# Kernel tuning notes

Hardware: AMD Instinct MI355X
Metric: run time of the kernel (lower is better)

## Reference

```python
import jax, jax.numpy as jnp
import numpy as np
import math

B, S, HID = 2, 4096, 2048
H, D, C = 16, 128, 256  # heads, head_dim, chunk (block) size
NC = S // C


def _build_slopes(n):
    # faithful port of MiniMaxText01LinearAttention._build_slope_tensor
    def p2(m):
        start = 2.0 ** (-(2.0 ** (-(math.log2(m) - 3))))
        return [start * (start ** i) for i in range(m)]
    if math.log2(n).is_integer():
        sl = p2(n)
    else:
        cp = 2 ** math.floor(math.log2(n))
        sl = p2(cp) + p2(2 * cp)[0::2][: n - cp]
    return np.asarray(sl, dtype=np.float32).reshape(n, 1, 1)


def setup_inputs() -> dict:
    key = jax.random.key(0)
    k1, k2, k3, k4 = jax.random.split(key, 4)
    x = jax.random.normal(k1, (B, S, HID), dtype=jnp.float32)
    w_qkv = jax.random.normal(k2, (HID, 3 * H * D), dtype=jnp.float32) * 0.02
    w_gate = jax.random.normal(k3, (HID, H * D), dtype=jnp.float32) * 0.02
    w_out = jax.random.normal(k4, (H * D, HID), dtype=jnp.float32) * 0.02
    slopes = jnp.asarray(_build_slopes(H))  # [H,1,1]
    return {"x": x, "w_qkv": w_qkv, "w_gate": w_gate, "w_out": w_out, "slopes": slopes}


def _to_chunks(t):
    # [B,S,H*D] -> [NC,B,H,C,D]
    return (t.reshape(B, S, H, D)
             .transpose(0, 2, 1, 3)          # [B,H,S,D]
             .reshape(B, H, NC, C, D)
             .transpose(2, 0, 1, 3, 4))      # [NC,B,H,C,D]


def _lightning_attn(q, k, v, slopes):
    # q,k,v: [NC,B,H,C,D]; slopes: [H,1,1]
    s = slopes
    pos = jnp.arange(C, dtype=jnp.float32)
    q_decay = jnp.exp(-s * (pos + 1.0).reshape(1, C, 1))        # [H,C,1]
    k_decay = jnp.exp(-s * (C - 1.0 - pos).reshape(1, C, 1))    # [H,C,1]
    idx = pos[:, None] - pos[None, :]                            # [C,C]
    diag_decay = jnp.where(idx >= 0, jnp.exp(-s * idx), 0.0)     # [H,C,C]
    block_decay = jnp.exp(-s * float(C))[None]                   # [1,H,1,1]

    def step(kv, qkv_c):
        qc, kc, vc = qkv_c  # each [B,H,C,D]
        # intra-chunk (causal, decayed)
        scores = jnp.einsum('bhid,bhjd->bhij', qc, kc) * diag_decay
        o = jnp.einsum('bhij,bhjd->bhid', scores, vc)
        # inter-chunk via recurrent state kv: [B,H,D,D]
        o = o + jnp.einsum('bhid,bhde->bhie', qc * q_decay, kv)
        kv = block_decay * kv + jnp.einsum('bhjd,bhje->bhde', kc * k_decay, vc)
        return kv, o

    kv0 = jnp.zeros((B, H, D, D), dtype=q.dtype)
    _, outs = jax.lax.scan(step, kv0, (q, k, v))  # outs: [NC,B,H,C,D]
    return (outs.transpose(1, 2, 0, 3, 4)          # [B,H,NC,C,D]
                .reshape(B, H, S, D)
                .transpose(0, 2, 1, 3)
                .reshape(B, S, H * D))


def reference(x, w_qkv, w_gate, w_out, slopes):
    qkv = jax.nn.silu(x @ w_qkv)                   # act on fused qkv (hidden_act=silu)
    q, k, v = jnp.split(qkv, 3, axis=-1)
    attn = _lightning_attn(_to_chunks(q), _to_chunks(k), _to_chunks(v), slopes)
    gate = jax.nn.sigmoid(x @ w_gate)              # output gate
    return (gate * attn) @ w_out
```

## Files before the change

kernel.cpp:

```cpp
#include <hip/hip_runtime.h>

typedef __bf16 bf16;
typedef __bf16 bf16x8 __attribute__((ext_vector_type(8)));
typedef __bf16 bf16x4 __attribute__((ext_vector_type(4)));
typedef float  f32x4  __attribute__((ext_vector_type(4)));

#define B_   2
#define S_   4096
#define HID_ 2048
#define H_   16
#define D_   128
#define C_   256
#define NC_  16
#define M_   (B_*S_)
#define K_   2048

typedef __attribute__((address_space(1))) const void gas_t;
typedef __attribute__((address_space(3))) void las_t;

__global__ void cvt_x_kernel(const float* __restrict__ x, bf16* __restrict__ xb) {
    int idx = (blockIdx.x * 256 + threadIdx.x) * 8;
    float4 f0 = *(const float4*)(x + idx);
    float4 f1 = *(const float4*)(x + idx + 4);
    bf16x8 o;
    o[0] = (bf16)f0.x; o[1] = (bf16)f0.y; o[2] = (bf16)f0.z; o[3] = (bf16)f0.w;
    o[4] = (bf16)f1.x; o[5] = (bf16)f1.y; o[6] = (bf16)f1.z; o[7] = (bf16)f1.w;
    *(bf16x8*)(xb + idx) = o;
}

__global__ void cvt_w_kernel(const float* __restrict__ wqkv,
                             const float* __restrict__ wgate,
                             const float* __restrict__ wout,
                             bf16* __restrict__ wT) {
    __shared__ float tile[32][33];
    int k0 = blockIdx.x * 32, n0 = blockIdx.y * 32;
    const float* src; int ld, col0;
    if (n0 < 6144)      { src = wqkv;  ld = 6144; col0 = n0; }
    else if (n0 < 8192) { src = wgate; ld = 2048; col0 = n0 - 6144; }
    else                { src = wout;  ld = 2048; col0 = n0 - 8192; }
    int tx = threadIdx.x, ty = threadIdx.y;
#pragma unroll
    for (int i = 0; i < 4; i++) {
        int kk = ty + i * 8;
        tile[kk][tx] = src[(size_t)(k0 + kk) * ld + col0 + tx];
    }
    __syncthreads();
#pragma unroll
    for (int i = 0; i < 4; i++) {
        int nn = ty + i * 8;
        wT[(size_t)(n0 + nn) * K_ + k0 + tx] = (bf16)tile[tx][nn];
    }
}

template <int MODE>
__global__ __launch_bounds__(256) void gemm_kernel(
        const bf16* __restrict__ A, const bf16* __restrict__ Bm,
        bf16* __restrict__ qo, bf16* __restrict__ ko,
        bf16* __restrict__ vo, bf16* __restrict__ go,
        float* __restrict__ out) {
    __shared__ __align__(16) bf16 As[128 * 32];
    __shared__ __align__(16) bf16 Bs[128 * 32];
    const int m0 = blockIdx.x * 128, n0 = blockIdx.y * 128;
    const int tid = threadIdx.x, lane = tid & 63, wid = tid >> 6;
    const int quad = lane >> 4, l15 = lane & 15;
    const int i0w = (wid >> 1) * 64, j0w = (wid & 1) * 64;
    f32x4 acc[4][4] = {};
    const int srow = tid >> 2, scol = (tid & 3) * 8;
    const bf16* Ag = A  + (size_t)(m0 + srow) * K_ + scol;
    const bf16* Bg = Bm + (size_t)(n0 + srow) * K_ + scol;
    const size_t rowskip = (size_t)64 * K_;
    bf16* AsDst = As + tid * 8;
    bf16* BsDst = Bs + tid * 8;

    for (int kb = 0; kb < K_; kb += 32) {
        __builtin_amdgcn_global_load_lds((gas_t*)(Ag + kb),           (las_t*)AsDst,          16, 0, 0);
        __builtin_amdgcn_global_load_lds((gas_t*)(Ag + kb + rowskip), (las_t*)(AsDst + 2048), 16, 0, 0);
        __builtin_amdgcn_global_load_lds((gas_t*)(Bg + kb),           (las_t*)BsDst,          16, 0, 0);
        __builtin_amdgcn_global_load_lds((gas_t*)(Bg + kb + rowskip), (las_t*)(BsDst + 2048), 16, 0, 0);
        __syncthreads();
        bf16x8 af[4], bfr[4];
#pragma unroll
        for (int t = 0; t < 4; t++)
            af[t] = *(const bf16x8*)&As[(i0w + t * 16 + l15) * 32 + quad * 8];
#pragma unroll
        for (int t = 0; t < 4; t++)
            bfr[t] = *(const bf16x8*)&Bs[(j0w + t * 16 + l15) * 32 + quad * 8];
#pragma unroll
        for (int ti = 0; ti < 4; ti++)
#pragma unroll
            for (int tj = 0; tj < 4; tj++)
                acc[ti][tj] = __builtin_amdgcn_mfma_f32_16x16x32_bf16(
                    af[ti], bfr[tj], acc[ti][tj], 0, 0, 0);
        __syncthreads();
    }

    if (MODE == 0) {
        bf16* outb = (n0 < 2048) ? qo : (n0 < 4096) ? ko : (n0 < 6144) ? vo : go;
        const bool silu = (n0 < 6144);
        const int cb = n0 & 2047;
#pragma unroll
        for (int ti = 0; ti < 4; ti++)
#pragma unroll
            for (int tj = 0; tj < 4; tj++)
#pragma unroll
                for (int r = 0; r < 4; r++) {
                    int row = m0 + i0w + ti * 16 + quad * 4 + r;
                    int col = cb + j0w + tj * 16 + l15;
                    float xv = acc[ti][tj][r];
                    float sg = 1.f / (1.f + __expf(-xv));
                    float av = silu ? xv * sg : sg;
                    outb[(size_t)row * 2048 + col] = (bf16)av;
                }
    } else {
#pragma unroll
        for (int ti = 0; ti < 4; ti++)
#pragma unroll
            for (int tj = 0; tj < 4; tj++)
#pragma unroll
                for (int r = 0; r < 4; r++) {
                    int row = m0 + i0w + ti * 16 + quad * 4 + r;
                    int col = n0 + j0w + tj * 16 + l15;
                    out[(size_t)row * 2048 + col] = acc[ti][tj][r];
                }
    }
}

__global__ void transpose_kernel(const bf16* __restrict__ kin,
                                 const bf16* __restrict__ vin,
                                 bf16* __restrict__ kT, bf16* __restrict__ vT) {
    __shared__ bf16 tile[64][65];
    int x0 = blockIdx.x * 64, d0 = blockIdx.y * 64;
    int z = blockIdx.z, arr = z >> 5, bh = z & 31, b = bh >> 4, h = bh & 15;
    const bf16* src = arr ? vin : kin;
    bf16* dst = arr ? vT : kT;
    int tx = threadIdx.x, ty = threadIdx.y;
#pragma unroll
    for (int r = 0; r < 16; r++) {
        int lr = ty * 16 + r;
        tile[lr][tx] = src[(size_t)(b * S_ + x0 + lr) * 2048 + h * 128 + d0 + tx];
    }
    __syncthreads();
#pragma unroll
    for (int r = 0; r < 16; r++) {
        int lr = ty * 16 + r;
        dst[(size_t)(bh * 128 + d0 + lr) * S_ + x0 + tx] = tile[tx][lr];
    }
}

__global__ __launch_bounds__(256) void pass_a_kernel(
        const bf16* __restrict__ kT, const bf16* __restrict__ vT,
        const float* __restrict__ slopes, bf16* __restrict__ KVT) {
    int c = blockIdx.x, bh = blockIdx.y;
    int tid = threadIdx.x, lane = tid & 63, wid = tid >> 6;
    int quad = lane >> 4, l15 = lane & 15;
    int e0 = (wid >> 1) * 64, d0 = (wid & 1) * 64;
    float s = slopes[bh & 15];
    float es = __expf(s);
    const bf16* vb = vT + (size_t)bh * 128 * S_ + c * 256;
    const bf16* kb = kT + (size_t)bh * 128 * S_ + c * 256;
    f32x4 acc[4][4] = {};
    for (int kbs = 0; kbs < 256; kbs += 32) {
        int j0 = kbs + quad * 8;
        float f[8];
        f[0] = __expf(-s * (float)(255 - j0));
#pragma unroll
        for (int jj = 1; jj < 8; jj++) f[jj] = f[jj - 1] * es;
        bf16x8 af[4], bfr[4];
#pragma unroll
        for (int t = 0; t < 4; t++)
            af[t] = *(const bf16x8*)(vb + (size_t)(e0 + t * 16 + l15) * S_ + j0);
#pragma unroll
        for (int t = 0; t < 4; t++) {
            bf16x8 raw = *(const bf16x8*)(kb + (size_t)(d0 + t * 16 + l15) * S_ + j0);
            bf16x8 sc;
#pragma unroll
            for (int jj = 0; jj < 8; jj++) sc[jj] = (bf16)((float)raw[jj] * f[jj]);
            bfr[t] = sc;
        }
#pragma unroll
        for (int ti = 0; ti < 4; ti++)
#pragma unroll
            for (int tj = 0; tj < 4; tj++)
                acc[ti][tj] = __builtin_amdgcn_mfma_f32_16x16x32_bf16(
                    af[ti], bfr[tj], acc[ti][tj], 0, 0, 0);
    }
    size_t base = ((size_t)c * 32 + bh) * 16384;
#pragma unroll
    for (int ti = 0; ti < 4; ti++)
#pragma unroll
        for (int tj = 0; tj < 4; tj++)
#pragma unroll
            for (int r = 0; r < 4; r++) {
                int e = e0 + ti * 16 + quad * 4 + r, d = d0 + tj * 16 + l15;
                KVT[base + (size_t)e * 128 + d] = (bf16)acc[ti][tj][r];
            }
}

__global__ void scan_kernel(const bf16* __restrict__ KVT,
                            const float* __restrict__ slopes,
                            bf16* __restrict__ stT) {
    int slice = blockIdx.x, bh = blockIdx.y;
    float s = slopes[bh & 15];
    float bd = __expf(-s * 256.f);
    size_t off = (size_t)slice * 1024 + threadIdx.x * 4;
    float kv0 = 0.f, kv1 = 0.f, kv2 = 0.f, kv3 = 0.f;
    for (int c = 0; c < 16; c++) {
        size_t idx = ((size_t)c * 32 + bh) * 16384 + off;
        bf16x4 st;
        st[0] = (bf16)kv0; st[1] = (bf16)kv1; st[2] = (bf16)kv2; st[3] = (bf16)kv3;
        *(bf16x4*)(stT + idx) = st;
        bf16x4 kvc = *(const bf16x4*)(KVT + idx);
        kv0 = bd * kv0 + (float)kvc[0];
        kv1 = bd * kv1 + (float)kvc[1];
        kv2 = bd * kv2 + (float)kvc[2];
        kv3 = bd * kv3 + (float)kvc[3];
    }
}

__global__ __launch_bounds__(256) void pass_c_kernel(
        const bf16* __restrict__ q, const bf16* __restrict__ kk,
        const bf16* __restrict__ vT, const bf16* __restrict__ stT,
        const bf16* __restrict__ gate, const float* __restrict__ slopes,
        bf16* __restrict__ og) {
    __shared__ __align__(16) bf16 P[256 * 72];
    __shared__ float dtab[257];
    int c = blockIdx.x, bh = blockIdx.y, b = bh >> 4, h = bh & 15;
    int tid = threadIdx.x, lane = tid & 63, wid = tid >> 6;
    int quad = lane >> 4, l15 = lane & 15;
    int i0 = wid * 64;
    float s = slopes[h];
    dtab[tid] = __expf(-s * (float)tid);
    if (tid == 0) dtab[256] = __expf(-s * 256.f);
    __syncthreads();
    const bf16* qb = q  + ((size_t)(b * S_ + c * 256)) * 2048 + h * 128;
    const bf16* kb = kk + ((size_t)(b * S_ + c * 256)) * 2048 + h * 128;
    const bf16* vb = vT + (size_t)bh * 128 * S_ + c * 256;
    const bf16* st = stT + ((size_t)c * 32 + bh) * 16384;
    f32x4 acc[4][8] = {};

    for (int kbs = 0; kbs < 128; kbs += 32) {
        bf16x8 af[4];
#pragma unroll
        for (int t = 0; t < 4; t++) {
            int i = i0 + t * 16 + l15;
            float qd = dtab[i + 1];
            bf16x8 raw = *(const bf16x8*)(qb + (size_t)i * 2048 + kbs + quad * 8);
            bf16x8 sc;
#pragma unroll
            for (int jj = 0; jj < 8; jj++) sc[jj] = (bf16)((float)raw[jj] * qd);
            af[t] = sc;
        }
#pragma unroll
        for (int te = 0; te < 8; te++) {
            bf16x8 bfr = *(const bf16x8*)(st + (size_t)(te * 16 + l15) * 128 + kbs + quad * 8);
#pragma unroll
            for (int t = 0; t < 4; t++)
                acc[t][te] = __builtin_amdgcn_mfma_f32_16x16x32_bf16(
                    af[t], bfr, acc[t][te], 0, 0, 0);
        }
    }

    for (int jt = 0; jt < 4; jt++) {
        f32x4 sacc[4][4] = {};
        for (int kbs = 0; kbs < 128; kbs += 32) {
            bf16x8 af[4], bkr[4];
#pragma unroll
            for (int t = 0; t < 4; t++)
                af[t] = *(const bf16x8*)(qb + (size_t)(i0 + t * 16 + l15) * 2048 + kbs + quad * 8);
#pragma unroll
            for (int t = 0; t < 4; t++)
                bkr[t] = *(const bf16x8*)(kb + (size_t)(jt * 64 + t * 16 + l15) * 2048 + kbs + quad * 8);
#pragma unroll
            for (int ti = 0; ti < 4; ti++)
#pragma unroll
                for (int tj = 0; tj < 4; tj++)
                    sacc[ti][tj] = __builtin_amdgcn_mfma_f32_16x16x32_bf16(
                        af[ti], bkr[tj], sacc[ti][tj], 0, 0, 0);
        }
#pragma unroll
        for (int ti = 0; ti < 4; ti++)
#pragma unroll
            for (int tj = 0; tj < 4; tj++)
#pragma unroll
                for (int r = 0; r < 4; r++) {
                    int i = i0 + ti * 16 + quad * 4 + r;
                    int j = jt * 64 + tj * 16 + l15;
                    int diff = i - j;
                    float pv = (diff >= 0) ? sacc[ti][tj][r] * dtab[diff] : 0.f;
                    P[i * 72 + tj * 16 + l15] = (bf16)pv;
                }
#pragma unroll
        for (int k2 = 0; k2 < 64; k2 += 32) {
            bf16x8 af[4];
#pragma unroll
            for (int t = 0; t < 4; t++)
                af[t] = *(const bf16x8*)&P[(i0 + t * 16 + l15) * 72 + k2 + quad * 8];
#pragma unroll
            for (int te = 0; te < 8; te++) {
                bf16x8 bfr = *(const bf16x8*)(vb + (size_t)(te * 16 + l15) * S_ + jt * 64 + k2 + quad * 8);
#pragma unroll
                for (int t = 0; t < 4; t++)
                    acc[t][te] = __builtin_amdgcn_mfma_f32_16x16x32_bf16(
                        af[t], bfr, acc[t][te], 0, 0, 0);
            }
        }
    }

    const bf16* gb = gate + ((size_t)(b * S_ + c * 256)) * 2048 + h * 128;
    bf16* ob = og + ((size_t)(b * S_ + c * 256)) * 2048 + h * 128;
#pragma unroll
    for (int ti = 0; ti < 4; ti++)
#pragma unroll
        for (int te = 0; te < 8; te++)
#pragma unroll
            for (int r = 0; r < 4; r++) {
                int i = i0 + ti * 16 + quad * 4 + r;
                int e = te * 16 + l15;
                float gv = (float)gb[(size_t)i * 2048 + e];
                ob[(size_t)i * 2048 + e] = (bf16)(acc[ti][te][r] * gv);
            }
}

extern "C" void kernel_launch(void* const* d_in, const int* in_sizes, int n_in,
                              void* d_out, int out_size, void* d_ws, size_t ws_size,
                              hipStream_t stream) {
    const float* x      = (const float*)d_in[0];
    const float* wqkv   = (const float*)d_in[1];
    const float* wgate  = (const float*)d_in[2];
    const float* wout   = (const float*)d_in[3];
    const float* slopes = (const float*)d_in[4];
    float* out = (float*)d_out;

    bf16* wT   = (bf16*)d_ws;
    bf16* xb   = wT   + (size_t)10240 * 2048;
    bf16* qb   = xb   + (size_t)8192 * 2048;
    bf16* kbuf = qb   + (size_t)8192 * 2048;
    bf16* vbuf = kbuf + (size_t)8192 * 2048;
    bf16* gbuf = vbuf + (size_t)8192 * 2048;
    bf16* kT   = xb;
    bf16* vT   = (bf16*)d_out;
    bf16* KVT  = vT + (size_t)32 * 128 * 4096;
    bf16* stT  = KVT + (size_t)16 * 32 * 16384;

    cvt_x_kernel<<<dim3(8192), dim3(256), 0, stream>>>(x, xb);
    cvt_w_kernel<<<dim3(64, 320), dim3(32, 8), 0, stream>>>(wqkv, wgate, wout, wT);
    gemm_kernel<0><<<dim3(64, 64), dim3(256), 0, stream>>>(
        xb, wT, qb, kbuf, vbuf, gbuf, (float*)nullptr);
    transpose_kernel<<<dim3(64, 2, 64), dim3(64, 4), 0, stream>>>(kbuf, vbuf, kT, vT);
    pass_a_kernel<<<dim3(16, 32), dim3(256), 0, stream>>>(kT, vT, slopes, KVT);
    scan_kernel<<<dim3(16, 32), dim3(256), 0, stream>>>(KVT, slopes, stT);
    pass_c_kernel<<<dim3(16, 32), dim3(256), 0, stream>>>(
        qb, kbuf, vT, stT, gbuf, slopes, vbuf);
    gemm_kernel<1><<<dim3(64, 16), dim3(256), 0, stream>>>(
        vbuf, wT + (size_t)8192 * 2048, nullptr, nullptr, nullptr, nullptr, out);
}
```

Measured before the change: 741.5 us.

## Merge convert kernels, swizzle GEMM LDS, fold k-decay, skip masked tiles in pass C

The x and weight conversion kernels are merged into one launch. The GEMM's LDS tiles get an XOR swizzle so fragment reads avoid bank conflicts. The k_decay scaling moves from pass A into the transpose that writes kT. Pass C now scales the query decay on the fp32 accumulator instead of the bf16 inputs, and interleaves rows across waves so each wave computes only the causal (jt<=ti) score tiles, which skips the fully masked upper-triangle work. The cost is a smaller per-wave P buffer and more loop-carried structure, plus slightly different rounding points.

```diff
diff --git a/kernel.cpp b/kernel.cpp
--- a/kernel.cpp
+++ b/kernel.cpp
@@ -18,27 +18,30 @@
 typedef __attribute__((address_space(1))) const void gas_t;
 typedef __attribute__((address_space(3))) void las_t;
 
-__global__ void cvt_x_kernel(const float* __restrict__ x, bf16* __restrict__ xb) {
-    int idx = (blockIdx.x * 256 + threadIdx.x) * 8;
-    float4 f0 = *(const float4*)(x + idx);
-    float4 f1 = *(const float4*)(x + idx + 4);
-    bf16x8 o;
-    o[0] = (bf16)f0.x; o[1] = (bf16)f0.y; o[2] = (bf16)f0.z; o[3] = (bf16)f0.w;
-    o[4] = (bf16)f1.x; o[5] = (bf16)f1.y; o[6] = (bf16)f1.z; o[7] = (bf16)f1.w;
-    *(bf16x8*)(xb + idx) = o;
-}
-
-__global__ void cvt_w_kernel(const float* __restrict__ wqkv,
-                             const float* __restrict__ wgate,
-                             const float* __restrict__ wout,
-                             bf16* __restrict__ wT) {
+__global__ void cvt_kernel(const float* __restrict__ x,
+                           const float* __restrict__ wqkv,
+                           const float* __restrict__ wgate,
+                           const float* __restrict__ wout,
+                           bf16* __restrict__ xb, bf16* __restrict__ wT) {
     __shared__ float tile[32][33];
-    int k0 = blockIdx.x * 32, n0 = blockIdx.y * 32;
+    int bid = blockIdx.x, tid = threadIdx.x;
+    if (bid < 8192) {
+        int idx = (bid * 256 + tid) * 8;
+        float4 f0 = *(const float4*)(x + idx);
+        float4 f1 = *(const float4*)(x + idx + 4);
+        bf16x8 o;
+        o[0] = (bf16)f0.x; o[1] = (bf16)f0.y; o[2] = (bf16)f0.z; o[3] = (bf16)f0.w;
+        o[4] = (bf16)f1.x; o[5] = (bf16)f1.y; o[6] = (bf16)f1.z; o[7] = (bf16)f1.w;
+        *(bf16x8*)(xb + idx) = o;
+        return;
+    }
+    bid -= 8192;
+    int k0 = (bid & 63) * 32, n0 = (bid >> 6) * 32;
     const float* src; int ld, col0;
     if (n0 < 6144)      { src = wqkv;  ld = 6144; col0 = n0; }
     else if (n0 < 8192) { src = wgate; ld = 2048; col0 = n0 - 6144; }
     else                { src = wout;  ld = 2048; col0 = n0 - 8192; }
-    int tx = threadIdx.x, ty = threadIdx.y;
+    int tx = tid & 31, ty = tid >> 5;
 #pragma unroll
     for (int i = 0; i < 4; i++) {
         int kk = ty + i * 8;
@@ -65,12 +68,14 @@
     const int quad = lane >> 4, l15 = lane & 15;
     const int i0w = (wid >> 1) * 64, j0w = (wid & 1) * 64;
     f32x4 acc[4][4] = {};
-    const int srow = tid >> 2, scol = (tid & 3) * 8;
-    const bf16* Ag = A  + (size_t)(m0 + srow) * K_ + scol;
-    const bf16* Bg = Bm + (size_t)(n0 + srow) * K_ + scol;
+    const int srow = tid >> 2;
+    const int sq = (tid & 3) ^ ((tid >> 3) & 3);
+    const bf16* Ag = A  + (size_t)(m0 + srow) * K_ + sq * 8;
+    const bf16* Bg = Bm + (size_t)(n0 + srow) * K_ + sq * 8;
     const size_t rowskip = (size_t)64 * K_;
     bf16* AsDst = As + tid * 8;
     bf16* BsDst = Bs + tid * 8;
+    const int slot = quad ^ ((l15 >> 1) & 3);
 
     for (int kb = 0; kb < K_; kb += 32) {
         __builtin_amdgcn_global_load_lds((gas_t*)(Ag + kb),           (las_t*)AsDst,          16, 0, 0);
@@ -81,10 +86,10 @@
         bf16x8 af[4], bfr[4];
 #pragma unroll
         for (int t = 0; t < 4; t++)
-            af[t] = *(const bf16x8*)&As[(i0w + t * 16 + l15) * 32 + quad * 8];
+            af[t] = *(const bf16x8*)&As[(i0w + t * 16 + l15) * 32 + slot * 8];
 #pragma unroll
         for (int t = 0; t < 4; t++)
-            bfr[t] = *(const bf16x8*)&Bs[(j0w + t * 16 + l15) * 32 + quad * 8];
+            bfr[t] = *(const bf16x8*)&Bs[(j0w + t * 16 + l15) * 32 + slot * 8];
 #pragma unroll
         for (int ti = 0; ti < 4; ti++)
 #pragma unroll
@@ -127,6 +132,7 @@
 
 __global__ void transpose_kernel(const bf16* __restrict__ kin,
                                  const bf16* __restrict__ vin,
+                                 const float* __restrict__ slopes,
                                  bf16* __restrict__ kT, bf16* __restrict__ vT) {
     __shared__ bf16 tile[64][65];
     int x0 = blockIdx.x * 64, d0 = blockIdx.y * 64;
@@ -134,6 +140,9 @@
     const bf16* src = arr ? vin : kin;
     bf16* dst = arr ? vT : kT;
     int tx = threadIdx.x, ty = threadIdx.y;
+    float fscale = 1.f;
+    if (arr == 0)
+        fscale = __expf(-slopes[h] * (float)(255 - ((x0 + tx) & 255)));
 #pragma unroll
     for (int r = 0; r < 16; r++) {
         int lr = ty * 16 + r;
@@ -143,40 +152,30 @@
 #pragma unroll
     for (int r = 0; r < 16; r++) {
         int lr = ty * 16 + r;
-        dst[(size_t)(bh * 128 + d0 + lr) * S_ + x0 + tx] = tile[tx][lr];
+        dst[(size_t)(bh * 128 + d0 + lr) * S_ + x0 + tx] =
+            (bf16)((float)tile[tx][lr] * fscale);
     }
 }
 
 __global__ __launch_bounds__(256) void pass_a_kernel(
         const bf16* __restrict__ kT, const bf16* __restrict__ vT,
-        const float* __restrict__ slopes, bf16* __restrict__ KVT) {
+        bf16* __restrict__ KVT) {
     int c = blockIdx.x, bh = blockIdx.y;
     int tid = threadIdx.x, lane = tid & 63, wid = tid >> 6;
     int quad = lane >> 4, l15 = lane & 15;
     int e0 = (wid >> 1) * 64, d0 = (wid & 1) * 64;
-    float s = slopes[bh & 15];
-    float es = __expf(s);
     const bf16* vb = vT + (size_t)bh * 128 * S_ + c * 256;
     const bf16* kb = kT + (size_t)bh * 128 * S_ + c * 256;
     f32x4 acc[4][4] = {};
     for (int kbs = 0; kbs < 256; kbs += 32) {
         int j0 = kbs + quad * 8;
-        float f[8];
-        f[0] = __expf(-s * (float)(255 - j0));
-#pragma unroll
-        for (int jj = 1; jj < 8; jj++) f[jj] = f[jj - 1] * es;
         bf16x8 af[4], bfr[4];
 #pragma unroll
         for (int t = 0; t < 4; t++)
             af[t] = *(const bf16x8*)(vb + (size_t)(e0 + t * 16 + l15) * S_ + j0);
 #pragma unroll
-        for (int t = 0; t < 4; t++) {
-            bf16x8 raw = *(const bf16x8*)(kb + (size_t)(d0 + t * 16 + l15) * S_ + j0);
-            bf16x8 sc;
-#pragma unroll
-            for (int jj = 0; jj < 8; jj++) sc[jj] = (bf16)((float)raw[jj] * f[jj]);
-            bfr[t] = sc;
-        }
+        for (int t = 0; t < 4; t++)
+            bfr[t] = *(const bf16x8*)(kb + (size_t)(d0 + t * 16 + l15) * S_ + j0);
 #pragma unroll
         for (int ti = 0; ti < 4; ti++)
 #pragma unroll
@@ -222,12 +221,11 @@
         const bf16* __restrict__ vT, const bf16* __restrict__ stT,
         const bf16* __restrict__ gate, const float* __restrict__ slopes,
         bf16* __restrict__ og) {
-    __shared__ __align__(16) bf16 P[256 * 72];
+    __shared__ __align__(16) bf16 P[4][16 * 72];
     __shared__ float dtab[257];
     int c = blockIdx.x, bh = blockIdx.y, b = bh >> 4, h = bh & 15;
     int tid = threadIdx.x, lane = tid & 63, wid = tid >> 6;
     int quad = lane >> 4, l15 = lane & 15;
-    int i0 = wid * 64;
     float s = slopes[h];
     dtab[tid] = __expf(-s * (float)tid);
     if (tid == 0) dtab[256] = __expf(-s * 256.f);
@@ -236,72 +234,67 @@
     const bf16* kb = kk + ((size_t)(b * S_ + c * 256)) * 2048 + h * 128;
     const bf16* vb = vT + (size_t)bh * 128 * S_ + c * 256;
     const bf16* st = stT + ((size_t)c * 32 + bh) * 16384;
+    bf16* Pw = &P[wid][0];
+    const int rbase = wid * 16;
     f32x4 acc[4][8] = {};
 
     for (int kbs = 0; kbs < 128; kbs += 32) {
         bf16x8 af[4];
 #pragma unroll
-        for (int t = 0; t < 4; t++) {
-            int i = i0 + t * 16 + l15;
-            float qd = dtab[i + 1];
-            bf16x8 raw = *(const bf16x8*)(qb + (size_t)i * 2048 + kbs + quad * 8);
-            bf16x8 sc;
-#pragma unroll
-            for (int jj = 0; jj < 8; jj++) sc[jj] = (bf16)((float)raw[jj] * qd);
-            af[t] = sc;
-        }
+        for (int ti = 0; ti < 4; ti++)
+            af[ti] = *(const bf16x8*)(qb + (size_t)(ti * 64 + rbase + l15) * 2048 + kbs + quad * 8);
 #pragma unroll
         for (int te = 0; te < 8; te++) {
             bf16x8 bfr = *(const bf16x8*)(st + (size_t)(te * 16 + l15) * 128 + kbs + quad * 8);
 #pragma unroll
-            for (int t = 0; t < 4; t++)
-                acc[t][te] = __builtin_amdgcn_mfma_f32_16x16x32_bf16(
-                    af[t], bfr, acc[t][te], 0, 0, 0);
+            for (int ti = 0; ti < 4; ti++)
+                acc[ti][te] = __builtin_amdgcn_mfma_f32_16x16x32_bf16(
+                    af[ti], bfr, acc[ti][te], 0, 0, 0);
         }
     }
-
-    for (int jt = 0; jt < 4; jt++) {
-        f32x4 sacc[4][4] = {};
-        for (int kbs = 0; kbs < 128; kbs += 32) {
-            bf16x8 af[4], bkr[4];
-#pragma unroll
-            for (int t = 0; t < 4; t++)
-                af[t] = *(const bf16x8*)(qb + (size_t)(i0 + t * 16 + l15) * 2048 + kbs + quad * 8);
-#pragma unroll
-            for (int t = 0; t < 4; t++)
-                bkr[t] = *(const bf16x8*)(kb + (size_t)(jt * 64 + t * 16 + l15) * 2048 + kbs + quad * 8);
-#pragma unroll
-            for (int ti = 0; ti < 4; ti++)
-#pragma unroll
-                for (int tj = 0; tj < 4; tj++)
-                    sacc[ti][tj] = __builtin_amdgcn_mfma_f32_16x16x32_bf16(
-                        af[ti], bkr[tj], sacc[ti][tj], 0, 0, 0);
-        }
-#pragma unroll
-        for (int ti = 0; ti < 4; ti++)
+#pragma unroll
+    for (int ti = 0; ti < 4; ti++) {
+        float qd[4];
+#pragma unroll
+        for (int r = 0; r < 4; r++) qd[r] = dtab[ti * 64 + rbase + quad * 4 + r + 1];
+#pragma unroll
+        for (int te = 0; te < 8; te++)
+#pragma unroll
+            for (int r = 0; r < 4; r++) acc[ti][te][r] *= qd[r];
+    }
+
+#pragma unroll
+    for (int ti = 0; ti < 4; ti++) {
+        for (int jt = 0; jt <= ti; jt++) {
+            f32x4 sacc[4] = {};
+            for (int kbs = 0; kbs < 128; kbs += 32) {
+                bf16x8 afq = *(const bf16x8*)(qb + (size_t)(ti * 64 + rbase + l15) * 2048 + kbs + quad * 8);
+#pragma unroll
+                for (int tj = 0; tj < 4; tj++) {
+                    bf16x8 bk = *(const bf16x8*)(kb + (size_t)(jt * 64 + tj * 16 + l15) * 2048 + kbs + quad * 8);
+                    sacc[tj] = __builtin_amdgcn_mfma_f32_16x16x32_bf16(
+                        afq, bk, sacc[tj], 0, 0, 0);
+                }
+            }
 #pragma unroll
             for (int tj = 0; tj < 4; tj++)
 #pragma unroll
                 for (int r = 0; r < 4; r++) {
-                    int i = i0 + ti * 16 + quad * 4 + r;
+                    int i = ti * 64 + rbase + quad * 4 + r;
                     int j = jt * 64 + tj * 16 + l15;
                     int diff = i - j;
-                    float pv = (diff >= 0) ? sacc[ti][tj][r] * dtab[diff] : 0.f;
-                    P[i * 72 + tj * 16 + l15] = (bf16)pv;
-                }
-#pragma unroll
-        for (int k2 = 0; k2 < 64; k2 += 32) {
-            bf16x8 af[4];
-#pragma unroll
-            for (int t = 0; t < 4; t++)
-                af[t] = *(const bf16x8*)&P[(i0 + t * 16 + l15) * 72 + k2 + quad * 8];
-#pragma unroll
-            for (int te = 0; te < 8; te++) {
-                bf16x8 bfr = *(const bf16x8*)(vb + (size_t)(te * 16 + l15) * S_ + jt * 64 + k2 + quad * 8);
-#pragma unroll
-                for (int t = 0; t < 4; t++)
-                    acc[t][te] = __builtin_amdgcn_mfma_f32_16x16x32_bf16(
-                        af[t], bfr, acc[t][te], 0, 0, 0);
+                    float pv = (diff >= 0) ? sacc[tj][r] * dtab[diff] : 0.f;
+                    Pw[(quad * 4 + r) * 72 + tj * 16 + l15] = (bf16)pv;
+                }
+#pragma unroll
+            for (int k2 = 0; k2 < 64; k2 += 32) {
+                bf16x8 afp = *(const bf16x8*)&Pw[l15 * 72 + k2 + quad * 8];
+#pragma unroll
+                for (int te = 0; te < 8; te++) {
+                    bf16x8 bv = *(const bf16x8*)(vb + (size_t)(te * 16 + l15) * S_ + jt * 64 + k2 + quad * 8);
+                    acc[ti][te] = __builtin_amdgcn_mfma_f32_16x16x32_bf16(
+                        afp, bv, acc[ti][te], 0, 0, 0);
+                }
             }
         }
     }
@@ -314,7 +307,7 @@
         for (int te = 0; te < 8; te++)
 #pragma unroll
             for (int r = 0; r < 4; r++) {
-                int i = i0 + ti * 16 + quad * 4 + r;
+                int i = ti * 64 + rbase + quad * 4 + r;
                 int e = te * 16 + l15;
                 float gv = (float)gb[(size_t)i * 2048 + e];
                 ob[(size_t)i * 2048 + e] = (bf16)(acc[ti][te][r] * gv);
@@ -342,12 +335,12 @@
     bf16* KVT  = vT + (size_t)32 * 128 * 4096;
     bf16* stT  = KVT + (size_t)16 * 32 * 16384;
 
-    cvt_x_kernel<<<dim3(8192), dim3(256), 0, stream>>>(x, xb);
-    cvt_w_kernel<<<dim3(64, 320), dim3(32, 8), 0, stream>>>(wqkv, wgate, wout, wT);
+    cvt_kernel<<<dim3(28672), dim3(256), 0, stream>>>(x, wqkv, wgate, wout, xb, wT);
     gemm_kernel<0><<<dim3(64, 64), dim3(256), 0, stream>>>(
         xb, wT, qb, kbuf, vbuf, gbuf, (float*)nullptr);
-    transpose_kernel<<<dim3(64, 2, 64), dim3(64, 4), 0, stream>>>(kbuf, vbuf, kT, vT);
-    pass_a_kernel<<<dim3(16, 32), dim3(256), 0, stream>>>(kT, vT, slopes, KVT);
+    transpose_kernel<<<dim3(64, 2, 64), dim3(64, 4), 0, stream>>>(
+        kbuf, vbuf, slopes, kT, vT);
+    pass_a_kernel<<<dim3(16, 32), dim3(256), 0, stream>>>(kT, vT, KVT);
     scan_kernel<<<dim3(16, 32), dim3(256), 0, stream>>>(KVT, slopes, stT);
     pass_c_kernel<<<dim3(16, 32), dim3(256), 0, stream>>>(
         qb, kbuf, vT, stT, gbuf, slopes, vbuf);
```

New measurement: 788.6 us. 6.4% more time.

## Widen GEMM K-tile with XOR-swizzled LDS, merge convert kernels, fold k-decay into transpose

Applied to the files above, without the earlier changes.

The GEMM kernel now stages a 64-wide K slice per iteration instead of 32, using an XOR swizzle on the LDS column slot so fragment reads avoid bank conflicts and half as many barriers run. The two fp32-to-bf16 conversion kernels are merged into one launch. The per-position k decay factor moves from pass_a into the K transpose, so pass_a loads already-scaled keys. This trades larger LDS use per block for fewer syncs, and the decay now rounds once in the transpose instead of in pass_a.

```diff
diff --git a/kernel.cpp b/kernel.cpp
--- a/kernel.cpp
+++ b/kernel.cpp
@@ -18,27 +18,30 @@
 typedef __attribute__((address_space(1))) const void gas_t;
 typedef __attribute__((address_space(3))) void las_t;
 
-__global__ void cvt_x_kernel(const float* __restrict__ x, bf16* __restrict__ xb) {
-    int idx = (blockIdx.x * 256 + threadIdx.x) * 8;
-    float4 f0 = *(const float4*)(x + idx);
-    float4 f1 = *(const float4*)(x + idx + 4);
-    bf16x8 o;
-    o[0] = (bf16)f0.x; o[1] = (bf16)f0.y; o[2] = (bf16)f0.z; o[3] = (bf16)f0.w;
-    o[4] = (bf16)f1.x; o[5] = (bf16)f1.y; o[6] = (bf16)f1.z; o[7] = (bf16)f1.w;
-    *(bf16x8*)(xb + idx) = o;
-}
-
-__global__ void cvt_w_kernel(const float* __restrict__ wqkv,
-                             const float* __restrict__ wgate,
-                             const float* __restrict__ wout,
-                             bf16* __restrict__ wT) {
+__global__ void cvt_kernel(const float* __restrict__ x,
+                           const float* __restrict__ wqkv,
+                           const float* __restrict__ wgate,
+                           const float* __restrict__ wout,
+                           bf16* __restrict__ xb, bf16* __restrict__ wT) {
     __shared__ float tile[32][33];
-    int k0 = blockIdx.x * 32, n0 = blockIdx.y * 32;
+    int bid = blockIdx.x, tid = threadIdx.x;
+    if (bid < 8192) {
+        int idx = (bid * 256 + tid) * 8;
+        float4 f0 = *(const float4*)(x + idx);
+        float4 f1 = *(const float4*)(x + idx + 4);
+        bf16x8 o;
+        o[0] = (bf16)f0.x; o[1] = (bf16)f0.y; o[2] = (bf16)f0.z; o[3] = (bf16)f0.w;
+        o[4] = (bf16)f1.x; o[5] = (bf16)f1.y; o[6] = (bf16)f1.z; o[7] = (bf16)f1.w;
+        *(bf16x8*)(xb + idx) = o;
+        return;
+    }
+    bid -= 8192;
+    int k0 = (bid & 63) * 32, n0 = (bid >> 6) * 32;
     const float* src; int ld, col0;
     if (n0 < 6144)      { src = wqkv;  ld = 6144; col0 = n0; }
     else if (n0 < 8192) { src = wgate; ld = 2048; col0 = n0 - 6144; }
     else                { src = wout;  ld = 2048; col0 = n0 - 8192; }
-    int tx = threadIdx.x, ty = threadIdx.y;
+    int tx = tid & 31, ty = tid >> 5;
 #pragma unroll
     for (int i = 0; i < 4; i++) {
         int kk = ty + i * 8;
@@ -58,39 +61,48 @@
         bf16* __restrict__ qo, bf16* __restrict__ ko,
         bf16* __restrict__ vo, bf16* __restrict__ go,
         float* __restrict__ out) {
-    __shared__ __align__(16) bf16 As[128 * 32];
-    __shared__ __align__(16) bf16 Bs[128 * 32];
+    __shared__ __align__(16) bf16 As[128 * 64];
+    __shared__ __align__(16) bf16 Bs[128 * 64];
     const int m0 = blockIdx.x * 128, n0 = blockIdx.y * 128;
     const int tid = threadIdx.x, lane = tid & 63, wid = tid >> 6;
     const int quad = lane >> 4, l15 = lane & 15;
     const int i0w = (wid >> 1) * 64, j0w = (wid & 1) * 64;
     f32x4 acc[4][4] = {};
-    const int srow = tid >> 2, scol = (tid & 3) * 8;
-    const bf16* Ag = A  + (size_t)(m0 + srow) * K_ + scol;
-    const bf16* Bg = Bm + (size_t)(n0 + srow) * K_ + scol;
-    const size_t rowskip = (size_t)64 * K_;
+    const int srow = tid >> 3;
+    const int sl = (tid & 7) ^ (srow & 7);
+    const bf16* Ag = A  + (size_t)(m0 + srow) * K_ + sl * 8;
+    const bf16* Bg = Bm + (size_t)(n0 + srow) * K_ + sl * 8;
     bf16* AsDst = As + tid * 8;
     bf16* BsDst = Bs + tid * 8;
-
-    for (int kb = 0; kb < K_; kb += 32) {
-        __builtin_amdgcn_global_load_lds((gas_t*)(Ag + kb),           (las_t*)AsDst,          16, 0, 0);
-        __builtin_amdgcn_global_load_lds((gas_t*)(Ag + kb + rowskip), (las_t*)(AsDst + 2048), 16, 0, 0);
-        __builtin_amdgcn_global_load_lds((gas_t*)(Bg + kb),           (las_t*)BsDst,          16, 0, 0);
-        __builtin_amdgcn_global_load_lds((gas_t*)(Bg + kb + rowskip), (las_t*)(BsDst + 2048), 16, 0, 0);
+    const int xr = l15 & 7;
+
+    for (int kb = 0; kb < K_; kb += 64) {
+#pragma unroll
+        for (int r = 0; r < 4; r++) {
+            __builtin_amdgcn_global_load_lds((gas_t*)(Ag + kb + (size_t)r * 32 * K_),
+                                             (las_t*)(AsDst + r * 2048), 16, 0, 0);
+            __builtin_amdgcn_global_load_lds((gas_t*)(Bg + kb + (size_t)r * 32 * K_),
+                                             (las_t*)(BsDst + r * 2048), 16, 0, 0);
+        }
         __syncthreads();
-        bf16x8 af[4], bfr[4];
-#pragma unroll
-        for (int t = 0; t < 4; t++)
-            af[t] = *(const bf16x8*)&As[(i0w + t * 16 + l15) * 32 + quad * 8];
-#pragma unroll
-        for (int t = 0; t < 4; t++)
-            bfr[t] = *(const bf16x8*)&Bs[(j0w + t * 16 + l15) * 32 + quad * 8];
-#pragma unroll
-        for (int ti = 0; ti < 4; ti++)
-#pragma unroll
-            for (int tj = 0; tj < 4; tj++)
-                acc[ti][tj] = __builtin_amdgcn_mfma_f32_16x16x32_bf16(
-                    af[ti], bfr[tj], acc[ti][tj], 0, 0, 0);
+        bf16x8 af[2][4], bfr[2][4];
+#pragma unroll
+        for (int s2 = 0; s2 < 2; s2++) {
+            const int slot = (s2 * 4 + quad) ^ xr;
+#pragma unroll
+            for (int t = 0; t < 4; t++) {
+                af[s2][t]  = *(const bf16x8*)&As[(i0w + t * 16 + l15) * 64 + slot * 8];
+                bfr[s2][t] = *(const bf16x8*)&Bs[(j0w + t * 16 + l15) * 64 + slot * 8];
+            }
+        }
+#pragma unroll
+        for (int s2 = 0; s2 < 2; s2++)
+#pragma unroll
+            for (int ti = 0; ti < 4; ti++)
+#pragma unroll
+                for (int tj = 0; tj < 4; tj++)
+                    acc[ti][tj] = __builtin_amdgcn_mfma_f32_16x16x32_bf16(
+                        af[s2][ti], bfr[s2][tj], acc[ti][tj], 0, 0, 0);
         __syncthreads();
     }
 
@@ -127,6 +139,7 @@
 
 __global__ void transpose_kernel(const bf16* __restrict__ kin,
                                  const bf16* __restrict__ vin,
+                                 const float* __restrict__ slopes,
                                  bf16* __restrict__ kT, bf16* __restrict__ vT) {
     __shared__ bf16 tile[64][65];
     int x0 = blockIdx.x * 64, d0 = blockIdx.y * 64;
@@ -134,6 +147,9 @@
     const bf16* src = arr ? vin : kin;
     bf16* dst = arr ? vT : kT;
     int tx = threadIdx.x, ty = threadIdx.y;
+    float fscale = 1.f;
+    if (arr == 0)
+        fscale = __expf(-slopes[h] * (float)(255 - ((x0 + tx) & 255)));
 #pragma unroll
     for (int r = 0; r < 16; r++) {
         int lr = ty * 16 + r;
@@ -143,40 +159,30 @@
 #pragma unroll
     for (int r = 0; r < 16; r++) {
         int lr = ty * 16 + r;
-        dst[(size_t)(bh * 128 + d0 + lr) * S_ + x0 + tx] = tile[tx][lr];
+        dst[(size_t)(bh * 128 + d0 + lr) * S_ + x0 + tx] =
+            (bf16)((float)tile[tx][lr] * fscale);
     }
 }
 
 __global__ __launch_bounds__(256) void pass_a_kernel(
         const bf16* __restrict__ kT, const bf16* __restrict__ vT,
-        const float* __restrict__ slopes, bf16* __restrict__ KVT) {
+        bf16* __restrict__ KVT) {
     int c = blockIdx.x, bh = blockIdx.y;
     int tid = threadIdx.x, lane = tid & 63, wid = tid >> 6;
     int quad = lane >> 4, l15 = lane & 15;
     int e0 = (wid >> 1) * 64, d0 = (wid & 1) * 64;
-    float s = slopes[bh & 15];
-    float es = __expf(s);
     const bf16* vb = vT + (size_t)bh * 128 * S_ + c * 256;
     const bf16* kb = kT + (size_t)bh * 128 * S_ + c * 256;
     f32x4 acc[4][4] = {};
     for (int kbs = 0; kbs < 256; kbs += 32) {
         int j0 = kbs + quad * 8;
-        float f[8];
-        f[0] = __expf(-s * (float)(255 - j0));
-#pragma unroll
-        for (int jj = 1; jj < 8; jj++) f[jj] = f[jj - 1] * es;
         bf16x8 af[4], bfr[4];
 #pragma unroll
         for (int t = 0; t < 4; t++)
             af[t] = *(const bf16x8*)(vb + (size_t)(e0 + t * 16 + l15) * S_ + j0);
 #pragma unroll
-        for (int t = 0; t < 4; t++) {
-            bf16x8 raw = *(const bf16x8*)(kb + (size_t)(d0 + t * 16 + l15) * S_ + j0);
-            bf16x8 sc;
-#pragma unroll
-            for (int jj = 0; jj < 8; jj++) sc[jj] = (bf16)((float)raw[jj] * f[jj]);
-            bfr[t] = sc;
-        }
+        for (int t = 0; t < 4; t++)
+            bfr[t] = *(const bf16x8*)(kb + (size_t)(d0 + t * 16 + l15) * S_ + j0);
 #pragma unroll
         for (int ti = 0; ti < 4; ti++)
 #pragma unroll
@@ -342,12 +348,12 @@
     bf16* KVT  = vT + (size_t)32 * 128 * 4096;
     bf16* stT  = KVT + (size_t)16 * 32 * 16384;
 
-    cvt_x_kernel<<<dim3(8192), dim3(256), 0, stream>>>(x, xb);
-    cvt_w_kernel<<<dim3(64, 320), dim3(32, 8), 0, stream>>>(wqkv, wgate, wout, wT);
+    cvt_kernel<<<dim3(28672), dim3(256), 0, stream>>>(x, wqkv, wgate, wout, xb, wT);
     gemm_kernel<0><<<dim3(64, 64), dim3(256), 0, stream>>>(
         xb, wT, qb, kbuf, vbuf, gbuf, (float*)nullptr);
-    transpose_kernel<<<dim3(64, 2, 64), dim3(64, 4), 0, stream>>>(kbuf, vbuf, kT, vT);
-    pass_a_kernel<<<dim3(16, 32), dim3(256), 0, stream>>>(kT, vT, slopes, KVT);
+    transpose_kernel<<<dim3(64, 2, 64), dim3(64, 4), 0, stream>>>(
+        kbuf, vbuf, slopes, kT, vT);
+    pass_a_kernel<<<dim3(16, 32), dim3(256), 0, stream>>>(kT, vT, KVT);
     scan_kernel<<<dim3(16, 32), dim3(256), 0, stream>>>(KVT, slopes, stT);
     pass_c_kernel<<<dim3(16, 32), dim3(256), 0, stream>>>(
         qb, kbuf, vT, stT, gbuf, slopes, vbuf);
```

New measurement: 692.7 us. 1.07x faster.
